# Kernel optimization log

Measured on AMD Instinct MI355X. Metric: run time of the kernel, lower is better.

Reference implementation:

```python
import jax, jax.numpy as jnp
import numpy as np

B, T, D_IN, D_PHYS, H, L, C = 64, 512, 256, 32, 512, 2, 11


def setup_inputs() -> dict:
    key = jax.random.key(0)
    ks = jax.random.split(key, 20)
    def w(k, shape, fan_in):
        return jax.random.normal(k, shape, dtype=jnp.float32) * (1.0 / np.sqrt(fan_in))
    return {
        "main_feats": jax.random.normal(ks[0], (B, T, D_IN), dtype=jnp.float32),
        "phys_feats": jax.random.normal(ks[1], (B, T, D_PHYS), dtype=jnp.float32),
        "mask": jnp.ones((B, T), dtype=jnp.bool_),
        # main_proj
        "Wp": w(ks[2], (H, D_IN), D_IN), "bp": jnp.zeros((H,), jnp.float32),
        # prev-token embedding
        "emb": jax.random.normal(ks[3], (C, H), dtype=jnp.float32),
        # LSTM layer 0 (input 2H) and layer 1 (input H), PyTorch gate order i,f,g,o
        "Wih0": w(ks[4], (4 * H, 2 * H), 2 * H), "Whh0": w(ks[5], (4 * H, H), H),
        "bih0": jnp.zeros((4 * H,), jnp.float32), "bhh0": jnp.zeros((4 * H,), jnp.float32),
        "Wih1": w(ks[6], (4 * H, H), H), "Whh1": w(ks[7], (4 * H, H), H),
        "bih1": jnp.zeros((4 * H,), jnp.float32), "bhh1": jnp.zeros((4 * H,), jnp.float32),
        # head: Linear(H+phys -> H), ReLU, Linear(H -> C)
        "W1": w(ks[8], (H, H + D_PHYS), H + D_PHYS), "b1": jnp.zeros((H,), jnp.float32),
        "W2": w(ks[9], (C, H), H), "b2": jnp.zeros((C,), jnp.float32),
    }


def _lstm_cell(x, h, c, Wih, Whh, bih, bhh):
    g = x @ Wih.T + bih + h @ Whh.T + bhh          # [b, 4H]
    i, f, gg, o = jnp.split(g, 4, axis=-1)          # PyTorch order i,f,g,o
    c2 = jax.nn.sigmoid(f) * c + jax.nn.sigmoid(i) * jnp.tanh(gg)
    h2 = jax.nn.sigmoid(o) * jnp.tanh(c2)
    return h2, c2


def reference(main_feats, phys_feats, mask, Wp, bp, emb,
              Wih0, Whh0, bih0, bhh0, Wih1, Whh1, bih1, bhh1,
              W1, b1, W2, b2):
    b = main_feats.shape[0]
    h = Whh0.shape[1]
    x_main = main_feats @ Wp.T + bp                 # [B,T,H]

    def step(carry, xs):
        h0, c0, h1, c1, prev = carry
        xm, ph = xs                                  # [B,H], [B,phys]
        x = jnp.concatenate([xm, emb[prev]], axis=-1)  # [B,2H]
        h0, c0 = _lstm_cell(x, h0, c0, Wih0, Whh0, bih0, bhh0)
        h1, c1 = _lstm_cell(h0, h1, c1, Wih1, Whh1, bih1, bhh1)
        z = jnp.concatenate([h1, ph], axis=-1)       # [B,H+phys]
        logits = jax.nn.relu(z @ W1.T + b1) @ W2.T + b2  # [B,C]
        prev = jnp.argmax(logits, axis=-1)
        return (h0, c0, h1, c1, prev), logits

    zeros = jnp.zeros((b, h), jnp.float32)
    carry0 = (zeros, zeros, zeros, zeros, jnp.zeros((b,), jnp.int32))
    xs = (x_main.swapaxes(0, 1), phys_feats.swapaxes(0, 1))  # time-major
    _, logits_t = jax.lax.scan(step, carry0, xs)             # [T,B,C]
    logits_all = logits_t.swapaxes(0, 1)                     # [B,T,C]
    attn = jnp.zeros(mask.shape, logits_all.dtype)
    return logits_all, jnp.zeros_like(logits_all), attn
```

## Files before the change

kernel.cpp:

```cpp
#include <hip/hip_runtime.h>

#define Tn   512
#define NWG  256
#define NTH  1024

#define OFF_WCOMB 0
#define OFF_BC0   524288
#define OFF_EMBG  526336
#define OFF_H0T   548864
#define OFF_H1T   (OFF_H0T + 65536)
#define OFF_C0T   (OFF_H1T + 65536)
#define OFF_C1T   (OFF_C0T + 32768)
#define OFF_BAR   (OFF_C1T + 32768)
#define OFF_ARR   (OFF_BAR + 32)
#define OFF_TAG1  (OFF_ARR + 8192)
#define OFF_PTAG  (OFF_TAG1 + 8192)
#define ZERO_END  (OFF_PTAG + 2048)
#define ZERO_WORDS (ZERO_END - OFF_H0T)
#define OFF_PBUF  ZERO_END
#define WS_WORDS  (OFF_PBUF + 704 * 256)

#define OUT_LOGITS_WORDS 360448
#define OUT_TAIL_WORDS   393216

__global__ void k_wcomb(const float* __restrict__ Wih0, const float* __restrict__ Wp,
                        const float* __restrict__ bp, const float* __restrict__ bih0,
                        const float* __restrict__ bhh0, float* __restrict__ ws) {
    int j = blockIdx.x;
    int k = threadIdx.x;
    const float* row = Wih0 + (long)j * 1024;
    float acc = 0.f;
    for (int h = 0; h < 512; ++h) acc = fmaf(row[h], Wp[h * 256 + k], acc);
    ws[OFF_WCOMB + j * 256 + k] = acc;
    __shared__ float s[256];
    s[k] = row[k] * bp[k] + row[256 + k] * bp[256 + k];
    __syncthreads();
    for (int st = 128; st > 0; st >>= 1) { if (k < st) s[k] += s[k + st]; __syncthreads(); }
    if (k == 0) ws[OFF_BC0 + j] = bih0[j] + bhh0[j] + s[0];
}

__global__ void k_embg(const float* __restrict__ emb, const float* __restrict__ Wih0,
                       float* __restrict__ ws) {
    int cls = blockIdx.x >> 3;
    int j = ((blockIdx.x & 7) << 8) + threadIdx.x;
    const float* er = emb + cls * 512;
    const float* wr = Wih0 + (long)j * 1024 + 512;
    float acc = 0.f;
    for (int h = 0; h < 512; ++h) acc = fmaf(er[h], wr[h], acc);
    ws[OFF_EMBG + cls * 2048 + j] = acc;
}

__global__ void k_zero(float* __restrict__ ws) {
    long i = (long)blockIdx.x * blockDim.x + threadIdx.x;
    if (i < ZERO_WORDS) ws[OFF_H0T + i] = 0.f;
}

struct MP {
    const float *mainf, *phys, *Whh0, *Wih1, *Whh1, *bih1, *bhh1, *W1, *b1, *W2, *b2;
    float* ws;
    float* out;
};

struct Seg {
    const float* act;
    long rs;
    int kmaj;
    int klen;
    const float* wgt;
    int wld;
    int wcol0;
    int coh;
};

__device__ __forceinline__ float sigm(float x) { return 1.f / (1.f + expf(-x)); }

__device__ __forceinline__ void coh_issue16(const float* p, float4& v) {
    asm volatile("global_load_dwordx4 %0, %1, off sc0 sc1" : "=&v"(v) : "v"(p));
}
__device__ __forceinline__ void vm_wait0() {
    asm volatile("s_waitcnt vmcnt(0)" ::: "memory");
}
__device__ __forceinline__ void coh_store(float* p, float v) {
    __hip_atomic_store(p, v, __ATOMIC_RELAXED, __HIP_MEMORY_SCOPE_AGENT);
}

__device__ __forceinline__ void resolve(int ch, int nch0, const Seg* sg, int& s, int& k0, int& kc) {
    if (ch < nch0) { s = 0; k0 = ch << 7; }
    else           { s = 1; k0 = (ch - nch0) << 7; }
    kc = sg[s].klen - k0; if (kc > 128) kc = 128;
}

template <int NRH>
__device__ __forceinline__ void comp_tile(const float (*at)[72], const float (*wv)[132],
                                          int rg, int q, int b4, float* acc) {
    float4 a0 = *(const float4*)&at[4 * q + 0][b4 << 2];
    float4 a1 = *(const float4*)&at[4 * q + 1][b4 << 2];
    float4 a2 = *(const float4*)&at[4 * q + 2][b4 << 2];
    float4 a3 = *(const float4*)&at[4 * q + 3][b4 << 2];
    #pragma unroll
    for (int jr = 0; jr < NRH; ++jr) {
        float4 w4 = *(const float4*)&wv[rg * NRH + jr][q << 2];
        acc[jr * 4 + 0] = fmaf(w4.x, a0.x, acc[jr * 4 + 0]);
        acc[jr * 4 + 0] = fmaf(w4.y, a1.x, acc[jr * 4 + 0]);
        acc[jr * 4 + 0] = fmaf(w4.z, a2.x, acc[jr * 4 + 0]);
        acc[jr * 4 + 0] = fmaf(w4.w, a3.x, acc[jr * 4 + 0]);
        acc[jr * 4 + 1] = fmaf(w4.x, a0.y, acc[jr * 4 + 1]);
        acc[jr * 4 + 1] = fmaf(w4.y, a1.y, acc[jr * 4 + 1]);
        acc[jr * 4 + 1] = fmaf(w4.z, a2.y, acc[jr * 4 + 1]);
        acc[jr * 4 + 1] = fmaf(w4.w, a3.y, acc[jr * 4 + 1]);
        acc[jr * 4 + 2] = fmaf(w4.x, a0.z, acc[jr * 4 + 2]);
        acc[jr * 4 + 2] = fmaf(w4.y, a1.z, acc[jr * 4 + 2]);
        acc[jr * 4 + 2] = fmaf(w4.z, a2.z, acc[jr * 4 + 2]);
        acc[jr * 4 + 2] = fmaf(w4.w, a3.z, acc[jr * 4 + 2]);
        acc[jr * 4 + 3] = fmaf(w4.x, a0.w, acc[jr * 4 + 3]);
        acc[jr * 4 + 3] = fmaf(w4.y, a1.w, acc[jr * 4 + 3]);
        acc[jr * 4 + 3] = fmaf(w4.z, a2.w, acc[jr * 4 + 3]);
        acc[jr * 4 + 3] = fmaf(w4.w, a3.w, acc[jr * 4 + 3]);
    }
}

template <int NR>
__device__ float mm_run(const Seg* sg, int j0, int jstride, int tid, int b,
                        float (*actA)[72], float (*actB)[72],
                        float (*wA)[132], float (*wB)[132], float* redw) {
    constexpr int NRH = NR / 2;
    constexpr int NA = NRH * 4;
    const int b4 = tid & 15;
    const int q  = (tid >> 4) & 31;
    const int rg = tid >> 9;
    const int nch0 = (sg[0].klen + 127) >> 7;
    const int nch = nch0 + ((sg[1].klen + 127) >> 7);
    const int nq0 = (nch + 1) >> 1;
    float acc[NA];
    #pragma unroll
    for (int i = 0; i < NA; ++i) acc[i] = 0.f;

    for (int it = 0; it < nq0; ++it) {
        const int chA = it, chB = nq0 + it;
        const bool hasB = chB < nch;
        int sA, kA, kcA; resolve(chA, nch0, sg, sA, kA, kcA);
        int sB = 0, kB = 0, kcB = 0;
        if (hasB) resolve(chB, nch0, sg, sB, kB, kcB);
        const Seg gA = sg[sA];
        const Seg gB = sg[sB];

        float4 va0, va1, vb0, vb1;
        bool fA0 = false, fA1 = false, fB0 = false, fB1 = false, coh = false;
        if (gA.kmaj) {
            int kk0 = tid >> 4, b4s = tid & 15;
            int kk1 = kk0 + 64;
            fA0 = kk0 < kcA; fA1 = kk1 < kcA;
            if (fA0) { const float* p = gA.act + ((long)(kA + kk0) << 6) + (b4s << 2);
                       if (gA.coh) { coh_issue16(p, va0); coh = true; } else va0 = *(const float4*)p; }
            if (fA1) { const float* p = gA.act + ((long)(kA + kk1) << 6) + (b4s << 2);
                       if (gA.coh) { coh_issue16(p, va1); coh = true; } else va1 = *(const float4*)p; }
        } else {
            int k40 = tid >> 6, bb = tid & 63;
            int k41 = k40 + 16;
            fA0 = (k40 << 2) < kcA; fA1 = (k41 << 2) < kcA;
            if (fA0) { const float* p = gA.act + (long)bb * gA.rs + kA + (k40 << 2);
                       if (gA.coh) { coh_issue16(p, va0); coh = true; } else va0 = *(const float4*)p; }
            if (fA1) { const float* p = gA.act + (long)bb * gA.rs + kA + (k41 << 2);
                       if (gA.coh) { coh_issue16(p, va1); coh = true; } else va1 = *(const float4*)p; }
        }
        if (hasB) {
            if (gB.kmaj) {
                int kk0 = tid >> 4, b4s = tid & 15;
                int kk1 = kk0 + 64;
                fB0 = kk0 < kcB; fB1 = kk1 < kcB;
                if (fB0) { const float* p = gB.act + ((long)(kB + kk0) << 6) + (b4s << 2);
                           if (gB.coh) { coh_issue16(p, vb0); coh = true; } else vb0 = *(const float4*)p; }
                if (fB1) { const float* p = gB.act + ((long)(kB + kk1) << 6) + (b4s << 2);
                           if (gB.coh) { coh_issue16(p, vb1); coh = true; } else vb1 = *(const float4*)p; }
            } else {
                int k40 = tid >> 6, bb = tid & 63;
                int k41 = k40 + 16;
                fB0 = (k40 << 2) < kcB; fB1 = (k41 << 2) < kcB;
                if (fB0) { const float* p = gB.act + (long)bb * gB.rs + kB + (k40 << 2);
                           if (gB.coh) { coh_issue16(p, vb0); coh = true; } else vb0 = *(const float4*)p; }
                if (fB1) { const float* p = gB.act + (long)bb * gB.rs + kB + (k41 << 2);
                           if (gB.coh) { coh_issue16(p, vb1); coh = true; } else vb1 = *(const float4*)p; }
            }
        }
        float wva = 0.f, wvb = 0.f;
        const int rw = tid >> 7, kkw = tid & 127;
        const bool wact = rw < NR;
        if (wact) {
            int j = (rw >> 1) * jstride + j0 + (rw & 1);
            if (kkw < kcA) wva = gA.wgt[(long)j * gA.wld + gA.wcol0 + kA + kkw];
            if (hasB && kkw < kcB) wvb = gB.wgt[(long)j * gB.wld + gB.wcol0 + kB + kkw];
        }
        if (coh) vm_wait0();
        if (gA.kmaj) {
            int kk0 = tid >> 4, b4s = tid & 15;
            if (fA0) *(float4*)&actA[kk0][b4s << 2] = va0;
            if (fA1) *(float4*)&actA[kk0 + 64][b4s << 2] = va1;
        } else {
            int k40 = tid >> 6, bb = tid & 63;
            if (fA0) { actA[(k40 << 2) + 0][bb] = va0.x; actA[(k40 << 2) + 1][bb] = va0.y;
                       actA[(k40 << 2) + 2][bb] = va0.z; actA[(k40 << 2) + 3][bb] = va0.w; }
            if (fA1) { int k41 = k40 + 16;
                       actA[(k41 << 2) + 0][bb] = va1.x; actA[(k41 << 2) + 1][bb] = va1.y;
                       actA[(k41 << 2) + 2][bb] = va1.z; actA[(k41 << 2) + 3][bb] = va1.w; }
        }
        if (hasB) {
            if (gB.kmaj) {
                int kk0 = tid >> 4, b4s = tid & 15;
                if (fB0) *(float4*)&actB[kk0][b4s << 2] = vb0;
                if (fB1) *(float4*)&actB[kk0 + 64][b4s << 2] = vb1;
            } else {
                int k40 = tid >> 6, bb = tid & 63;
                if (fB0) { actB[(k40 << 2) + 0][bb] = vb0.x; actB[(k40 << 2) + 1][bb] = vb0.y;
                           actB[(k40 << 2) + 2][bb] = vb0.z; actB[(k40 << 2) + 3][bb] = vb0.w; }
                if (fB1) { int k41 = k40 + 16;
                           actB[(k41 << 2) + 0][bb] = vb1.x; actB[(k41 << 2) + 1][bb] = vb1.y;
                           actB[(k41 << 2) + 2][bb] = vb1.z; actB[(k41 << 2) + 3][bb] = vb1.w; }
            }
        }
        if (wact) {
            if (kkw < kcA) wA[rw][kkw] = wva;
            if (hasB && kkw < kcB) wB[rw][kkw] = wvb;
        }
        __syncthreads();
        {
            int s_, k0c, kc; resolve(chA, nch0, sg, s_, k0c, kc);
            if (4 * q < kc) comp_tile<NRH>(actA, wA, rg, q, b4, acc);
        }
        if (hasB) {
            int s_, k0c, kc; resolve(chB, nch0, sg, s_, k0c, kc);
            if (4 * q < kc) comp_tile<NRH>(actB, wB, rg, q, b4, acc);
        }
        __syncthreads();
    }
    #pragma unroll
    for (int i = 0; i < NA; ++i) {
        acc[i] += __shfl_xor(acc[i], 16);
        acc[i] += __shfl_xor(acc[i], 32);
    }
    const int wv_ = tid >> 6, lane = tid & 63;
    if (lane < 16) {
        float* dst = redw + (((rg * 8 + (wv_ & 7)) * 16) + b4) * NA;
        #pragma unroll
        for (int i = 0; i < NA; ++i) dst[i] = acc[i];
    }
    __syncthreads();
    float out = 0.f;
    if (tid < NR * 64) {
        const int rr = tid >> 6, bb = tid & 63;
        const int rg2 = rr / NRH, jr2 = rr % NRH;
        #pragma unroll
        for (int p_ = 0; p_ < 8; ++p_)
            out += redw[(((rg2 * 8 + p_) * 16) + (bb >> 2)) * NA + jr2 * 4 + (bb & 3)];
    }
    __syncthreads();
    return out;
}

__device__ __forceinline__ void gsync(int* done, int* arr, int w, int gen) {
    vm_wait0();
    __syncthreads();
    const int tid = threadIdx.x;
    if (tid == 0)
        __hip_atomic_store(&arr[w * 32], gen, __ATOMIC_RELAXED, __HIP_MEMORY_SCOPE_AGENT);
    if (w == 0) {
        if (tid < NWG) {
            int v;
            do {
                __builtin_amdgcn_s_sleep(1);
                v = __hip_atomic_load(&arr[tid * 32], __ATOMIC_RELAXED, __HIP_MEMORY_SCOPE_AGENT);
            } while (v < gen);
        }
        __syncthreads();
        if (tid == 0)
            __hip_atomic_store(done, gen, __ATOMIC_RELAXED, __HIP_MEMORY_SCOPE_AGENT);
    } else {
        if (tid == 0) {
            int v;
            do {
                __builtin_amdgcn_s_sleep(2);
                v = __hip_atomic_load(done, __ATOMIC_RELAXED, __HIP_MEMORY_SCOPE_AGENT);
            } while (v < gen);
        }
    }
    __syncthreads();
}

__global__ void __launch_bounds__(NTH, 4) k_main(MP p) {
    float* ws = p.ws;
    const float* Wcomb = ws + OFF_WCOMB;
    const float* bc0v  = ws + OFF_BC0;
    const float* embg  = ws + OFF_EMBG;
    float* h0T = ws + OFF_H0T;
    float* h1T = ws + OFF_H1T;
    float* c0T = ws + OFF_C0T;
    float* c1T = ws + OFF_C1T;
    float* pbuf = ws + OFF_PBUF;
    int* done = (int*)(ws + OFF_BAR);
    int* arr  = (int*)(ws + OFF_ARR);
    int* tag1 = (int*)(ws + OFF_TAG1);
    int* ptag = (int*)(ws + OFF_PTAG);

    __shared__ float actA[128][72], actB[128][72];
    __shared__ float wA[8][132], wB[8][132];
    __shared__ float redw[2 * 8 * 16 * 16];
    __shared__ float red[8][64];
    __shared__ float rrow[2][64];
    __shared__ float slog[11];
    __shared__ int prevlS[64];

    const int w = blockIdx.x, tid = threadIdx.x, b = tid & 63;
    int gen = 0;

    for (int t = 0; t <= Tn; ++t) {
        const int cur = t & 1, prv = cur ^ 1;

        if (t >= 1) {
            Seg sg[2];
            sg[0] = { h1T + prv * 32768, 0, 1, 512, p.W1, 544, 0, 1 };
            sg[1] = { p.phys + (long)(t - 1) * 32, (long)Tn * 32, 0, 32, p.W1, 544, 512, 0 };
            float ha = mm_run<2>(sg, 2 * w, 512, tid, b, actA, actB, wA, wB, redw);
            if (tid < 128) {
                float rr = ha + p.b1[2 * w + (tid >> 6)];
                rrow[tid >> 6][b] = rr > 0.f ? rr : 0.f;
            }
            __syncthreads();
            if (tid < 64) {
                float r0 = rrow[0][b], r1 = rrow[1][b];
                #pragma unroll
                for (int cc = 0; cc < 11; ++cc)
                    coh_store(&pbuf[((long)(b * 11 + cc) << 8) + w],
                              fmaf(r0, p.W2[cc * 512 + 2 * w], r1 * p.W2[cc * 512 + 2 * w + 1]));
            }
            if (tid == 0) {
                vm_wait0();
                __hip_atomic_store(&tag1[w * 32], t, __ATOMIC_RELAXED, __HIP_MEMORY_SCOPE_AGENT);
            }

            if (w < 64) {
                if (tid < 256) {
                    int v;
                    do {
                        __builtin_amdgcn_s_sleep(1);
                        v = __hip_atomic_load(&tag1[tid * 32], __ATOMIC_RELAXED, __HIP_MEMORY_SCOPE_AGENT);
                    } while (v < t);
                }
                __syncthreads();
                if (tid < 704) {
                    int cc = tid >> 6, i = tid & 63;
                    const float* pb = pbuf + ((long)(w * 11 + cc) << 8);
                    float s = 0.f;
                    #pragma unroll
                    for (int u = 0; u < 4; ++u)
                        s += __hip_atomic_load(&pb[i + (u << 6)], __ATOMIC_RELAXED, __HIP_MEMORY_SCOPE_AGENT);
                    #pragma unroll
                    for (int off = 32; off; off >>= 1) s += __shfl_down(s, off);
                    if (i == 0) slog[cc] = s + p.b2[cc];
                }
                __syncthreads();
                if (tid == 0) {
                    float best = -3.4e38f; int am = 0;
                    #pragma unroll
                    for (int cc = 0; cc < 11; ++cc) {
                        float v = slog[cc];
                        p.out[(long)w * (Tn * 11) + (long)(t - 1) * 11 + cc] = v;
                        if (v > best) { best = v; am = cc; }
                    }
                    __hip_atomic_store(&ptag[w * 32], (t << 4) | am, __ATOMIC_RELAXED, __HIP_MEMORY_SCOPE_AGENT);
                }
            }
        }
        if (t == Tn) break;

        {
            Seg sg[2];
            sg[0] = { p.mainf + (long)t * 256, (long)Tn * 256, 0, 256, Wcomb, 256, 0, 0 };
            sg[1] = { h0T + prv * 32768, 0, 1, 512, p.Whh0, 512, 0, 1 };
            float ga = mm_run<8>(sg, 2 * w, 512, tid, b, actA, actB, wA, wB, redw);
            if (tid < 64) {
                if (t >= 1) {
                    int v;
                    do {
                        __builtin_amdgcn_s_sleep(1);
                        v = __hip_atomic_load(&ptag[tid * 32], __ATOMIC_RELAXED, __HIP_MEMORY_SCOPE_AGENT);
                    } while ((v >> 4) < t);
                    prevlS[tid] = v & 15;
                } else prevlS[tid] = 0;
            }
            __syncthreads();
            if (tid < 512) {
                int rr_ = tid >> 6;
                int jrow = (rr_ >> 1) * 512 + 2 * w + (rr_ & 1);
                int pv = prevlS[b];
                red[rr_][b] = ga + bc0v[jrow] + embg[pv * 2048 + jrow];
            }
            __syncthreads();
            if (tid < 128) {
                int jj = tid >> 6, k = 2 * w + jj;
                float g0 = red[jj][b], g1 = red[2 + jj][b], g2 = red[4 + jj][b], g3 = red[6 + jj][b];
                float ci = c0T[k * 64 + b];
                float cn = sigm(g1) * ci + sigm(g0) * tanhf(g2);
                c0T[k * 64 + b] = cn;
                coh_store(&h0T[cur * 32768 + k * 64 + b], sigm(g3) * tanhf(cn));
            }
        }
        gsync(done, arr, w, ++gen);

        {
            Seg sg[2];
            sg[0] = { h0T + cur * 32768, 0, 1, 512, p.Wih1, 512, 0, 1 };
            sg[1] = { h1T + prv * 32768, 0, 1, 512, p.Whh1, 512, 0, 1 };
            float ga = mm_run<8>(sg, 2 * w, 512, tid, b, actA, actB, wA, wB, redw);
            __syncthreads();
            if (tid < 512) {
                int rr_ = tid >> 6;
                int jrow = (rr_ >> 1) * 512 + 2 * w + (rr_ & 1);
                red[rr_][b] = ga + p.bih1[jrow] + p.bhh1[jrow];
            }
            __syncthreads();
            if (tid < 128) {
                int jj = tid >> 6, k = 2 * w + jj;
                float g0 = red[jj][b], g1 = red[2 + jj][b], g2 = red[4 + jj][b], g3 = red[6 + jj][b];
                float ci = c1T[k * 64 + b];
                float cn = sigm(g1) * ci + sigm(g0) * tanhf(g2);
                c1T[k * 64 + b] = cn;
                coh_store(&h1T[cur * 32768 + k * 64 + b], sigm(g3) * tanhf(cn));
            }
        }
        gsync(done, arr, w, ++gen);
    }
}

extern "C" void kernel_launch(void* const* d_in, const int* in_sizes, int n_in,
                              void* d_out, int out_size, void* d_ws, size_t ws_size,
                              hipStream_t stream) {
    const float* mainf = (const float*)d_in[0];
    const float* phys  = (const float*)d_in[1];
    const float* Wp   = (const float*)d_in[3];
    const float* bp   = (const float*)d_in[4];
    const float* emb  = (const float*)d_in[5];
    const float* Wih0 = (const float*)d_in[6];
    const float* Whh0 = (const float*)d_in[7];
    const float* bih0 = (const float*)d_in[8];
    const float* bhh0 = (const float*)d_in[9];
    const float* Wih1 = (const float*)d_in[10];
    const float* Whh1 = (const float*)d_in[11];
    const float* bih1 = (const float*)d_in[12];
    const float* bhh1 = (const float*)d_in[13];
    const float* W1   = (const float*)d_in[14];
    const float* b1   = (const float*)d_in[15];
    const float* W2   = (const float*)d_in[16];
    const float* b2   = (const float*)d_in[17];
    float* out = (float*)d_out;
    float* ws  = (float*)d_ws;

    (void)hipMemsetAsync(out + OUT_LOGITS_WORDS, 0, (size_t)OUT_TAIL_WORDS * 4, stream);

    k_wcomb<<<2048, 256, 0, stream>>>(Wih0, Wp, bp, bih0, bhh0, ws);
    k_embg<<<88, 256, 0, stream>>>(emb, Wih0, ws);
    k_zero<<<(ZERO_WORDS + 255) / 256, 256, 0, stream>>>(ws);

    MP p{ mainf, phys, Whh0, Wih1, Whh1, bih1, bhh1, W1, b1, W2, b2, ws, out };
    k_main<<<NWG, NTH, 0, stream>>>(p);
}
```

Measured before the change: 19.51 ms.

## Repartition persistent LSTM kernel over hidden-unit groups and batch quarters

Changes the work split across the 256 persistent workgroups. Each workgroup now owns 8 hidden units and 16 batch rows, where before it owned 2 hidden units and all 64 batch rows. The goal is to cut per-block redundant loads of the activation tile and use wider float4 weight loads, with more weight rows per block, for better reuse. The reduction, the head partial-sum layout (64 partials per class instead of 256) and the argmax/tag handshakes are rewritten to match. In exchange, each block now streams 4x more weight rows and the head's cross-block dependency pattern changes.

```diff
diff --git a/kernel.cpp b/kernel.cpp
--- a/kernel.cpp
+++ b/kernel.cpp
@@ -91,7 +91,7 @@
 }
 
 template <int NRH>
-__device__ __forceinline__ void comp_tile(const float (*at)[72], const float (*wv)[132],
+__device__ __forceinline__ void comp_tile(const float (*at)[20], const float (*wv)[132],
                                           int rg, int q, int b4, float* acc) {
     float4 a0 = *(const float4*)&at[4 * q + 0][b4 << 2];
     float4 a1 = *(const float4*)&at[4 * q + 1][b4 << 2];
@@ -119,18 +119,18 @@
     }
 }
 
-template <int NR>
-__device__ float mm_run(const Seg* sg, int j0, int jstride, int tid, int b,
-                        float (*actA)[72], float (*actB)[72],
-                        float (*wA)[132], float (*wB)[132], float* redw) {
-    constexpr int NRH = NR / 2;
+template <int NR, int NRH>
+__device__ void mm_run(const Seg* sg, int j0, int jstride, int bq, int tid,
+                       float (*actA)[20], float (*actB)[20],
+                       float (*wA)[132], float (*wB)[132],
+                       float* redw, float* redf) {
     constexpr int NA = NRH * 4;
-    const int b4 = tid & 15;
-    const int q  = (tid >> 4) & 31;
-    const int rg = tid >> 9;
+    const int b4 = tid & 3;
+    const int q  = (tid >> 2) & 31;
+    const int rg = tid >> 7;
     const int nch0 = (sg[0].klen + 127) >> 7;
-    const int nch = nch0 + ((sg[1].klen + 127) >> 7);
-    const int nq0 = (nch + 1) >> 1;
+    const int nch  = nch0 + ((sg[1].klen + 127) >> 7);
+    const int nq0  = (nch + 1) >> 1;
     float acc[NA];
     #pragma unroll
     for (int i = 0; i < NA; ++i) acc[i] = 0.f;
@@ -144,116 +144,90 @@
         const Seg gA = sg[sA];
         const Seg gB = sg[sB];
 
-        float4 va0, va1, vb0, vb1;
-        bool fA0 = false, fA1 = false, fB0 = false, fB1 = false, coh = false;
-        if (gA.kmaj) {
-            int kk0 = tid >> 4, b4s = tid & 15;
-            int kk1 = kk0 + 64;
-            fA0 = kk0 < kcA; fA1 = kk1 < kcA;
-            if (fA0) { const float* p = gA.act + ((long)(kA + kk0) << 6) + (b4s << 2);
-                       if (gA.coh) { coh_issue16(p, va0); coh = true; } else va0 = *(const float4*)p; }
-            if (fA1) { const float* p = gA.act + ((long)(kA + kk1) << 6) + (b4s << 2);
-                       if (gA.coh) { coh_issue16(p, va1); coh = true; } else va1 = *(const float4*)p; }
-        } else {
-            int k40 = tid >> 6, bb = tid & 63;
-            int k41 = k40 + 16;
-            fA0 = (k40 << 2) < kcA; fA1 = (k41 << 2) < kcA;
-            if (fA0) { const float* p = gA.act + (long)bb * gA.rs + kA + (k40 << 2);
-                       if (gA.coh) { coh_issue16(p, va0); coh = true; } else va0 = *(const float4*)p; }
-            if (fA1) { const float* p = gA.act + (long)bb * gA.rs + kA + (k41 << 2);
-                       if (gA.coh) { coh_issue16(p, va1); coh = true; } else va1 = *(const float4*)p; }
-        }
-        if (hasB) {
-            if (gB.kmaj) {
-                int kk0 = tid >> 4, b4s = tid & 15;
-                int kk1 = kk0 + 64;
-                fB0 = kk0 < kcB; fB1 = kk1 < kcB;
-                if (fB0) { const float* p = gB.act + ((long)(kB + kk0) << 6) + (b4s << 2);
-                           if (gB.coh) { coh_issue16(p, vb0); coh = true; } else vb0 = *(const float4*)p; }
-                if (fB1) { const float* p = gB.act + ((long)(kB + kk1) << 6) + (b4s << 2);
-                           if (gB.coh) { coh_issue16(p, vb1); coh = true; } else vb1 = *(const float4*)p; }
+        const int abuf = tid >> 9;
+        const int st   = tid & 511;
+        const Seg* gS  = abuf ? &gB : &gA;
+        const int  kS  = abuf ? kB : kA;
+        const int  kcS = abuf ? kcB : kcA;
+        const bool bufOK = abuf ? hasB : true;
+        float4 av;
+        bool fAct = false;
+        if (bufOK) {
+            if (gS->kmaj) {
+                int kk = st >> 2, b4f = st & 3;
+                if (kk < kcS) {
+                    const float* pp = gS->act + ((long)(kS + kk) << 6) + (bq << 4) + (b4f << 2);
+                    fAct = true;
+                    if (gS->coh) coh_issue16(pp, av); else av = *(const float4*)pp;
+                }
             } else {
-                int k40 = tid >> 6, bb = tid & 63;
-                int k41 = k40 + 16;
-                fB0 = (k40 << 2) < kcB; fB1 = (k41 << 2) < kcB;
-                if (fB0) { const float* p = gB.act + (long)bb * gB.rs + kB + (k40 << 2);
-                           if (gB.coh) { coh_issue16(p, vb0); coh = true; } else vb0 = *(const float4*)p; }
-                if (fB1) { const float* p = gB.act + (long)bb * gB.rs + kB + (k41 << 2);
-                           if (gB.coh) { coh_issue16(p, vb1); coh = true; } else vb1 = *(const float4*)p; }
-            }
-        }
-        float wva = 0.f, wvb = 0.f;
-        const int rw = tid >> 7, kkw = tid & 127;
-        const bool wact = rw < NR;
-        if (wact) {
-            int j = (rw >> 1) * jstride + j0 + (rw & 1);
-            if (kkw < kcA) wva = gA.wgt[(long)j * gA.wld + gA.wcol0 + kA + kkw];
-            if (hasB && kkw < kcB) wvb = gB.wgt[(long)j * gB.wld + gB.wcol0 + kB + kkw];
-        }
-        if (coh) vm_wait0();
-        if (gA.kmaj) {
-            int kk0 = tid >> 4, b4s = tid & 15;
-            if (fA0) *(float4*)&actA[kk0][b4s << 2] = va0;
-            if (fA1) *(float4*)&actA[kk0 + 64][b4s << 2] = va1;
-        } else {
-            int k40 = tid >> 6, bb = tid & 63;
-            if (fA0) { actA[(k40 << 2) + 0][bb] = va0.x; actA[(k40 << 2) + 1][bb] = va0.y;
-                       actA[(k40 << 2) + 2][bb] = va0.z; actA[(k40 << 2) + 3][bb] = va0.w; }
-            if (fA1) { int k41 = k40 + 16;
-                       actA[(k41 << 2) + 0][bb] = va1.x; actA[(k41 << 2) + 1][bb] = va1.y;
-                       actA[(k41 << 2) + 2][bb] = va1.z; actA[(k41 << 2) + 3][bb] = va1.w; }
-        }
-        if (hasB) {
-            if (gB.kmaj) {
-                int kk0 = tid >> 4, b4s = tid & 15;
-                if (fB0) *(float4*)&actB[kk0][b4s << 2] = vb0;
-                if (fB1) *(float4*)&actB[kk0 + 64][b4s << 2] = vb1;
+                int k4 = st >> 4, bb = st & 15;
+                if ((k4 << 2) < kcS) {
+                    const float* pp = gS->act + (long)(bq * 16 + bb) * gS->rs + kS + (k4 << 2);
+                    fAct = true;
+                    if (gS->coh) coh_issue16(pp, av); else av = *(const float4*)pp;
+                }
+            }
+        }
+        float4 wva, wvb;
+        bool fWA = false, fWB = false;
+        const int rw = tid >> 5, kq = tid & 31;
+        if (rw < NR) {
+            int j = (rw >> 3) * jstride + j0 + (rw & 7);
+            if ((kq << 2) < kcA) {
+                wva = *(const float4*)(gA.wgt + (long)j * gA.wld + gA.wcol0 + kA + (kq << 2));
+                fWA = true;
+            }
+            if (hasB && (kq << 2) < kcB) {
+                wvb = *(const float4*)(gB.wgt + (long)j * gB.wld + gB.wcol0 + kB + (kq << 2));
+                fWB = true;
+            }
+        }
+        vm_wait0();
+        if (fAct) {
+            float (*dst)[20] = abuf ? actB : actA;
+            if (gS->kmaj) {
+                int kk = st >> 2, b4f = st & 3;
+                *(float4*)&dst[kk][b4f << 2] = av;
             } else {
-                int k40 = tid >> 6, bb = tid & 63;
-                if (fB0) { actB[(k40 << 2) + 0][bb] = vb0.x; actB[(k40 << 2) + 1][bb] = vb0.y;
-                           actB[(k40 << 2) + 2][bb] = vb0.z; actB[(k40 << 2) + 3][bb] = vb0.w; }
-                if (fB1) { int k41 = k40 + 16;
-                           actB[(k41 << 2) + 0][bb] = vb1.x; actB[(k41 << 2) + 1][bb] = vb1.y;
-                           actB[(k41 << 2) + 2][bb] = vb1.z; actB[(k41 << 2) + 3][bb] = vb1.w; }
-            }
-        }
-        if (wact) {
-            if (kkw < kcA) wA[rw][kkw] = wva;
-            if (hasB && kkw < kcB) wB[rw][kkw] = wvb;
-        }
+                int k4 = st >> 4, bb = st & 15;
+                dst[(k4 << 2) + 0][bb] = av.x; dst[(k4 << 2) + 1][bb] = av.y;
+                dst[(k4 << 2) + 2][bb] = av.z; dst[(k4 << 2) + 3][bb] = av.w;
+            }
+        }
+        if (fWA) *(float4*)&wA[rw][kq << 2] = wva;
+        if (fWB) *(float4*)&wB[rw][kq << 2] = wvb;
         __syncthreads();
-        {
-            int s_, k0c, kc; resolve(chA, nch0, sg, s_, k0c, kc);
-            if (4 * q < kc) comp_tile<NRH>(actA, wA, rg, q, b4, acc);
-        }
-        if (hasB) {
-            int s_, k0c, kc; resolve(chB, nch0, sg, s_, k0c, kc);
-            if (4 * q < kc) comp_tile<NRH>(actB, wB, rg, q, b4, acc);
-        }
+        if (4 * q < kcA) comp_tile<NRH>(actA, wA, rg, q, b4, acc);
+        if (hasB && 4 * q < kcB) comp_tile<NRH>(actB, wB, rg, q, b4, acc);
         __syncthreads();
     }
     #pragma unroll
     for (int i = 0; i < NA; ++i) {
+        acc[i] += __shfl_xor(acc[i], 4);
+        acc[i] += __shfl_xor(acc[i], 8);
         acc[i] += __shfl_xor(acc[i], 16);
         acc[i] += __shfl_xor(acc[i], 32);
     }
-    const int wv_ = tid >> 6, lane = tid & 63;
-    if (lane < 16) {
-        float* dst = redw + (((rg * 8 + (wv_ & 7)) * 16) + b4) * NA;
+    const int wv5 = tid >> 6, lane = tid & 63;
+    const int q4 = wv5 & 1, rgw = wv5 >> 1;
+    if (q4 == 1 && lane < 4) {
+        const int base = (rgw * 4 + lane) * 17;
         #pragma unroll
-        for (int i = 0; i < NA; ++i) dst[i] = acc[i];
+        for (int i = 0; i < NA; ++i) redw[base + i] = acc[i];
     }
     __syncthreads();
-    float out = 0.f;
-    if (tid < NR * 64) {
-        const int rr = tid >> 6, bb = tid & 63;
-        const int rg2 = rr / NRH, jr2 = rr % NRH;
+    if (q4 == 0 && lane < 4) {
+        const int base = (rgw * 4 + lane) * 17;
         #pragma unroll
-        for (int p_ = 0; p_ < 8; ++p_)
-            out += redw[(((rg2 * 8 + p_) * 16) + (bb >> 2)) * NA + jr2 * 4 + (bb & 3)];
+        for (int i = 0; i < NA; ++i) acc[i] += redw[base + i];
+        #pragma unroll
+        for (int jr = 0; jr < NRH; ++jr)
+            #pragma unroll
+            for (int jb = 0; jb < 4; ++jb)
+                redf[(rgw * NRH + jr) * 17 + lane * 4 + jb] = acc[jr * 4 + jb];
     }
     __syncthreads();
-    return out;
 }
 
 __device__ __forceinline__ void gsync(int* done, int* arr, int w, int gen) {
@@ -300,15 +274,16 @@
     int* tag1 = (int*)(ws + OFF_TAG1);
     int* ptag = (int*)(ws + OFF_PTAG);
 
-    __shared__ float actA[128][72], actB[128][72];
-    __shared__ float wA[8][132], wB[8][132];
-    __shared__ float redw[2 * 8 * 16 * 16];
-    __shared__ float red[8][64];
-    __shared__ float rrow[2][64];
+    __shared__ float actA[128][20], actB[128][20];
+    __shared__ float wA[32][132], wB[32][132];
+    __shared__ float redw[8 * 4 * 17];
+    __shared__ float redf[32 * 17];
+    __shared__ float rrowS[8][17];
     __shared__ float slog[11];
-    __shared__ int prevlS[64];
-
-    const int w = blockIdx.x, tid = threadIdx.x, b = tid & 63;
+    __shared__ int prevlS[16];
+
+    const int w = blockIdx.x, tid = threadIdx.x;
+    const int kg = w >> 2, bq = w & 3;
     int gen = 0;
 
     for (int t = 0; t <= Tn; ++t) {
@@ -318,43 +293,45 @@
             Seg sg[2];
             sg[0] = { h1T + prv * 32768, 0, 1, 512, p.W1, 544, 0, 1 };
             sg[1] = { p.phys + (long)(t - 1) * 32, (long)Tn * 32, 0, 32, p.W1, 544, 512, 0 };
-            float ha = mm_run<2>(sg, 2 * w, 512, tid, b, actA, actB, wA, wB, redw);
+            mm_run<8, 1>(sg, kg * 8, 0, bq, tid, actA, actB, wA, wB, redw, redf);
             if (tid < 128) {
-                float rr = ha + p.b1[2 * w + (tid >> 6)];
-                rrow[tid >> 6][b] = rr > 0.f ? rr : 0.f;
+                int rr = tid >> 4, bb = tid & 15;
+                float hv = redf[rr * 17 + bb] + p.b1[kg * 8 + rr];
+                rrowS[rr][bb] = hv > 0.f ? hv : 0.f;
             }
             __syncthreads();
-            if (tid < 64) {
-                float r0 = rrow[0][b], r1 = rrow[1][b];
+            if (tid < 176) {
+                int bb = tid / 11, cc = tid - bb * 11;
+                float s = 0.f;
                 #pragma unroll
-                for (int cc = 0; cc < 11; ++cc)
-                    coh_store(&pbuf[((long)(b * 11 + cc) << 8) + w],
-                              fmaf(r0, p.W2[cc * 512 + 2 * w], r1 * p.W2[cc * 512 + 2 * w + 1]));
-            }
-            if (tid == 0) {
-                vm_wait0();
+                for (int r = 0; r < 8; ++r)
+                    s = fmaf(rrowS[r][bb], p.W2[cc * 512 + kg * 8 + r], s);
+                int b = bq * 16 + bb;
+                coh_store(&pbuf[(long)(b * 11 + cc) * 64 + kg], s);
+            }
+            vm_wait0();
+            __syncthreads();
+            if (tid == 0)
                 __hip_atomic_store(&tag1[w * 32], t, __ATOMIC_RELAXED, __HIP_MEMORY_SCOPE_AGENT);
-            }
-
-            if (w < 64) {
-                if (tid < 256) {
+
+            if (bq == 0) {
+                const int b = kg;
+                if (tid < 64) {
                     int v;
                     do {
                         __builtin_amdgcn_s_sleep(1);
-                        v = __hip_atomic_load(&tag1[tid * 32], __ATOMIC_RELAXED, __HIP_MEMORY_SCOPE_AGENT);
+                        v = __hip_atomic_load(&tag1[(tid * 4 + (b >> 4)) * 32],
+                                              __ATOMIC_RELAXED, __HIP_MEMORY_SCOPE_AGENT);
                     } while (v < t);
                 }
                 __syncthreads();
                 if (tid < 704) {
-                    int cc = tid >> 6, i = tid & 63;
-                    const float* pb = pbuf + ((long)(w * 11 + cc) << 8);
-                    float s = 0.f;
-                    #pragma unroll
-                    for (int u = 0; u < 4; ++u)
-                        s += __hip_atomic_load(&pb[i + (u << 6)], __ATOMIC_RELAXED, __HIP_MEMORY_SCOPE_AGENT);
+                    int cc = tid >> 6, kgi = tid & 63;
+                    float s = __hip_atomic_load(&pbuf[(long)(b * 11 + cc) * 64 + kgi],
+                                                __ATOMIC_RELAXED, __HIP_MEMORY_SCOPE_AGENT);
                     #pragma unroll
                     for (int off = 32; off; off >>= 1) s += __shfl_down(s, off);
-                    if (i == 0) slog[cc] = s + p.b2[cc];
+                    if (kgi == 0) slog[cc] = s + p.b2[cc];
                 }
                 __syncthreads();
                 if (tid == 0) {
@@ -362,10 +339,11 @@
                     #pragma unroll
                     for (int cc = 0; cc < 11; ++cc) {
                         float v = slog[cc];
-                        p.out[(long)w * (Tn * 11) + (long)(t - 1) * 11 + cc] = v;
+                        p.out[(long)b * (Tn * 11) + (long)(t - 1) * 11 + cc] = v;
                         if (v > best) { best = v; am = cc; }
                     }
-                    __hip_atomic_store(&ptag[w * 32], (t << 4) | am, __ATOMIC_RELAXED, __HIP_MEMORY_SCOPE_AGENT);
+                    __hip_atomic_store(&ptag[b * 32], (t << 4) | am,
+                                       __ATOMIC_RELAXED, __HIP_MEMORY_SCOPE_AGENT);
                 }
             }
         }
@@ -375,28 +353,32 @@
             Seg sg[2];
             sg[0] = { p.mainf + (long)t * 256, (long)Tn * 256, 0, 256, Wcomb, 256, 0, 0 };
             sg[1] = { h0T + prv * 32768, 0, 1, 512, p.Whh0, 512, 0, 1 };
-            float ga = mm_run<8>(sg, 2 * w, 512, tid, b, actA, actB, wA, wB, redw);
-            if (tid < 64) {
+            mm_run<32, 4>(sg, kg * 8, 512, bq, tid, actA, actB, wA, wB, redw, redf);
+            if (tid < 16) {
                 if (t >= 1) {
                     int v;
                     do {
                         __builtin_amdgcn_s_sleep(1);
-                        v = __hip_atomic_load(&ptag[tid * 32], __ATOMIC_RELAXED, __HIP_MEMORY_SCOPE_AGENT);
+                        v = __hip_atomic_load(&ptag[(bq * 16 + tid) * 32],
+                                              __ATOMIC_RELAXED, __HIP_MEMORY_SCOPE_AGENT);
                     } while ((v >> 4) < t);
                     prevlS[tid] = v & 15;
                 } else prevlS[tid] = 0;
             }
             __syncthreads();
             if (tid < 512) {
-                int rr_ = tid >> 6;
-                int jrow = (rr_ >> 1) * 512 + 2 * w + (rr_ & 1);
-                int pv = prevlS[b];
-                red[rr_][b] = ga + bc0v[jrow] + embg[pv * 2048 + jrow];
+                int rr = tid >> 4, bb = tid & 15;
+                int jrow = (rr >> 3) * 512 + kg * 8 + (rr & 7);
+                redf[rr * 17 + bb] += bc0v[jrow] + embg[prevlS[bb] * 2048 + jrow];
             }
             __syncthreads();
             if (tid < 128) {
-                int jj = tid >> 6, k = 2 * w + jj;
-                float g0 = red[jj][b], g1 = red[2 + jj][b], g2 = red[4 + jj][b], g3 = red[6 + jj][b];
+                int jj = tid >> 4, bb = tid & 15;
+                int k = kg * 8 + jj, b = bq * 16 + bb;
+                float g0 = redf[jj * 17 + bb];
+                float g1 = redf[(8 + jj) * 17 + bb];
+                float g2 = redf[(16 + jj) * 17 + bb];
+                float g3 = redf[(24 + jj) * 17 + bb];
                 float ci = c0T[k * 64 + b];
                 float cn = sigm(g1) * ci + sigm(g0) * tanhf(g2);
                 c0T[k * 64 + b] = cn;
@@ -409,17 +391,20 @@
             Seg sg[2];
             sg[0] = { h0T + cur * 32768, 0, 1, 512, p.Wih1, 512, 0, 1 };
             sg[1] = { h1T + prv * 32768, 0, 1, 512, p.Whh1, 512, 0, 1 };
-            float ga = mm_run<8>(sg, 2 * w, 512, tid, b, actA, actB, wA, wB, redw);
-            __syncthreads();
+            mm_run<32, 4>(sg, kg * 8, 512, bq, tid, actA, actB, wA, wB, redw, redf);
             if (tid < 512) {
-                int rr_ = tid >> 6;
-                int jrow = (rr_ >> 1) * 512 + 2 * w + (rr_ & 1);
-                red[rr_][b] = ga + p.bih1[jrow] + p.bhh1[jrow];
+                int rr = tid >> 4, bb = tid & 15;
+                int jrow = (rr >> 3) * 512 + kg * 8 + (rr & 7);
+                redf[rr * 17 + bb] += p.bih1[jrow] + p.bhh1[jrow];
             }
             __syncthreads();
             if (tid < 128) {
-                int jj = tid >> 6, k = 2 * w + jj;
-                float g0 = red[jj][b], g1 = red[2 + jj][b], g2 = red[4 + jj][b], g3 = red[6 + jj][b];
+                int jj = tid >> 4, bb = tid & 15;
+                int k = kg * 8 + jj, b = bq * 16 + bb;
+                float g0 = redf[jj * 17 + bb];
+                float g1 = redf[(8 + jj) * 17 + bb];
+                float g2 = redf[(16 + jj) * 17 + bb];
+                float g3 = redf[(24 + jj) * 17 + bb];
                 float ci = c1T[k * 64 + b];
                 float cn = sigm(g1) * ci + sigm(g0) * tanhf(g2);
                 c1T[k * 64 + b] = cn;
```

Measured after the change: 22.23 ms. 13.9% more time.
